# Optimization experiments

Measured on AMD Instinct MI355X. Metric: run time of the kernel, lower is better.

The kernel has to match this reference:

```python
import jax, jax.numpy as jnp
import numpy as np

DIM = 768
HEADS = 12
HEAD_DIM = DIM // HEADS
SEQ = 196
BATCH = 64
SCALE = HEAD_DIM ** -0.5


def setup_inputs() -> dict:
    key = jax.random.key(0)
    ks = jax.random.split(key, 5)
    x = jax.random.normal(ks[0], (BATCH, SEQ, DIM), dtype=jnp.float32)
    W_qkv = jax.random.normal(ks[1], (DIM, 3 * DIM), dtype=jnp.float32) * (DIM ** -0.5)
    static_a = jax.random.truncated_normal(ks[2], -2.0, 2.0, (1, HEADS, SEQ, SEQ), dtype=jnp.float32)
    W_proj = jax.random.normal(ks[3], (DIM, DIM), dtype=jnp.float32) * (DIM ** -0.5)
    b_proj = jnp.zeros((DIM,), dtype=jnp.float32)
    return {"x": x, "W_qkv": W_qkv, "static_a": static_a, "W_proj": W_proj, "b_proj": b_proj}


def reference(x, W_qkv, static_a, W_proj, b_proj):
    B, N, C = x.shape
    qkv = (x @ W_qkv).reshape(B, N, 3, HEADS, HEAD_DIM)
    qkv = jnp.transpose(qkv, (2, 0, 3, 1, 4))  # [3, B, H, N, D]
    q, k, v = qkv[0], qkv[1], qkv[2]
    attn = jnp.einsum('bhnd,bhmd->bhnm', q, k) * SCALE
    attn = jax.nn.softmax(attn, axis=-1) + static_a  # post-softmax additive bias
    out = jnp.einsum('bhnm,bhmd->bhnd', attn, v)  # [B, H, N, D]
    out = jnp.transpose(out, (0, 2, 1, 3)).reshape(B, N, C)
    return out @ W_proj + b_proj
```

## Files before the change

kernel.cpp:

```cpp
#include <hip/hip_runtime.h>
#include <stdint.h>

#define DIM 768
#define HEADS 12
#define SEQ 196
#define BATCH 64
#define NTOK (BATCH*SEQ)
#define SCALE 0.125f

using short8  = __attribute__((ext_vector_type(8))) short;
using short4v = __attribute__((ext_vector_type(4))) short;
using float4v = __attribute__((ext_vector_type(4))) float;
using ushort4v = __attribute__((ext_vector_type(4))) unsigned short;

static __device__ __forceinline__ unsigned short f2bf(float f) {
  union { float f; unsigned u; } v; v.f = f;
  unsigned u = v.u;
  u += 0x7fffu + ((u >> 16) & 1u);
  return (unsigned short)(u >> 16);
}

#if defined(__has_builtin)
#if __has_builtin(__builtin_amdgcn_global_load_lds)
#define HAS_GLL 1
#endif
#endif

static __device__ __forceinline__ void gll16(const unsigned short* g, unsigned short* l) {
#ifdef HAS_GLL
  __builtin_amdgcn_global_load_lds(
      (const __attribute__((address_space(1))) void*)g,
      (__attribute__((address_space(3))) void*)l, 16, 0, 0);
#else
  const int lane = threadIdx.x & 63;
  *(short8*)(l + lane * 8) = *(const short8*)g;
#endif
}

__global__ __launch_bounds__(256) void cast_x_kernel(const float* __restrict__ in,
                                                     unsigned short* __restrict__ out) {
  int i = blockIdx.x * 256 + threadIdx.x;
  float4 v = ((const float4*)in)[i];
  ushort4v o;
  o.x = f2bf(v.x); o.y = f2bf(v.y); o.z = f2bf(v.z); o.w = f2bf(v.w);
  ((ushort4v*)out)[i] = o;
}

__global__ __launch_bounds__(256) void transpose_cast_kernel(const float* __restrict__ in,
                                                             unsigned short* __restrict__ out,
                                                             int R, int C) {
  __shared__ float tile[32][33];
  int c0 = blockIdx.x * 32, r0 = blockIdx.y * 32;
  int tx = threadIdx.x, ty = threadIdx.y;
  for (int i = 0; i < 32; i += 8)
    tile[ty + i][tx] = in[(size_t)(r0 + ty + i) * C + c0 + tx];
  __syncthreads();
  for (int i = 0; i < 32; i += 8)
    out[(size_t)(c0 + ty + i) * R + r0 + tx] = f2bf(tile[tx][ty + i]);
}

template <int MODE>
__global__ __launch_bounds__(256) void gemm_kernel(const unsigned short* __restrict__ A,
                                                   const unsigned short* __restrict__ Bt,
                                                   const float* __restrict__ bias,
                                                   unsigned short* __restrict__ outQKV,
                                                   float* __restrict__ outF) {
  constexpr int K = 768;
  __shared__ __align__(16) unsigned short Als[128 * 32];
  __shared__ __align__(16) unsigned short Bls[128 * 32];
  const int tid = threadIdx.x;
  const int wid = tid >> 6, lane = tid & 63;
  const int s = lane & 15, q = lane >> 4;
  const int wr = wid >> 1, wc = wid & 1;
  const int m0 = blockIdx.y * 128;
  const int n0 = blockIdx.x * 128;

  float4v acc[4][4];
  for (int i = 0; i < 4; i++)
    for (int j = 0; j < 4; j++) acc[i][j] = (float4v){0.f, 0.f, 0.f, 0.f};

  const int srow = lane >> 2;
  const int scol = (lane & 3) * 8;

  for (int kt = 0; kt < K; kt += 32) {
    const unsigned short* ga = A  + (size_t)(m0 + wid * 32 + srow) * K + kt + scol;
    const unsigned short* gb = Bt + (size_t)(n0 + wid * 32 + srow) * K + kt + scol;
    unsigned short* la = &Als[wid * 32 * 32];
    unsigned short* lb = &Bls[wid * 32 * 32];
    gll16(ga,           la);
    gll16(ga + 16 * K,  la + 16 * 32);
    gll16(gb,           lb);
    gll16(gb + 16 * K,  lb + 16 * 32);
    __syncthreads();

    short8 af[4], bf[4];
    for (int i = 0; i < 4; i++)
      af[i] = *(const short8*)&Als[(wr * 64 + i * 16 + s) * 32 + q * 8];
    for (int j = 0; j < 4; j++)
      bf[j] = *(const short8*)&Bls[(wc * 64 + j * 16 + s) * 32 + q * 8];
    for (int i = 0; i < 4; i++)
      for (int j = 0; j < 4; j++)
        acc[i][j] = __builtin_amdgcn_mfma_f32_16x16x32_bf16(af[i], bf[j], acc[i][j], 0, 0, 0);
    __syncthreads();
  }

  for (int i = 0; i < 4; i++) {
    int mbase = m0 + wr * 64 + i * 16 + q * 4;
    for (int j = 0; j < 4; j++) {
      int ng = n0 + wc * 64 + j * 16 + s;
      if (MODE == 0) {
        int t = ng / 768, rem = ng % 768;
        int h = rem >> 6, d = rem & 63;
        for (int r = 0; r < 4; r++) {
          int mg = mbase + r;
          int b = mg / 196, ns = mg - b * 196;
          size_t off = ((size_t)((t * BATCH + b) * HEADS + h) * SEQ + ns) * 64 + d;
          outQKV[off] = f2bf(acc[i][j][r]);
        }
      } else {
        float bv = bias[ng];
        for (int r = 0; r < 4; r++)
          outF[(size_t)(mbase + r) * 768 + ng] = acc[i][j][r] + bv;
      }
    }
  }
}

__global__ __launch_bounds__(256) void attn_kernel(const unsigned short* __restrict__ qkv,
                                                   const float* __restrict__ static_a,
                                                   unsigned short* __restrict__ outA) {
  constexpr int WV = 228;
  __shared__ __align__(16) unsigned short Vt[64 * WV];
  const int tid = threadIdx.x, wid = tid >> 6, lane = tid & 63;
  const int s = lane & 15, q = lane >> 4;
  const int bh = blockIdx.x;
  const int b = bh / 12, h = bh % 12;
  const size_t slab = (size_t)SEQ * 64;
  const unsigned short* Qb = qkv + (size_t)(0 * BATCH * HEADS + bh) * slab;
  const unsigned short* Kb = qkv + (size_t)(1 * BATCH * HEADS + bh) * slab;
  const unsigned short* Vb = qkv + (size_t)(2 * BATCH * HEADS + bh) * slab;

  {
    const int ms = tid & 63;
    const int d0 = (tid >> 6) * 16;
    for (int mb = 0; mb < 4; ++mb) {
      int m = mb * 64 + ms;
      if (m < 224) {
        if (m < 196) {
          short8 v0 = *(const short8*)&Vb[(size_t)m * 64 + d0];
          short8 v1 = *(const short8*)&Vb[(size_t)m * 64 + d0 + 8];
          for (int j = 0; j < 8; j++) Vt[(d0 + j) * WV + m] = (unsigned short)v0[j];
          for (int j = 0; j < 8; j++) Vt[(d0 + 8 + j) * WV + m] = (unsigned short)v1[j];
        } else {
          for (int j = 0; j < 16; j++) Vt[(d0 + j) * WV + m] = 0;
        }
      }
    }
  }
  __syncthreads();

  const int pmbase = (s >> 2) * 8 + (s & 3);

  for (int qt = wid; qt < 13; qt += 4) {
    const int n0 = qt * 16;
    const int nq = n0 + s;
    const int nql = nq > 195 ? 195 : nq;
    short8 qf0 = *(const short8*)&Qb[(size_t)nql * 64 + q * 8];
    short8 qf1 = *(const short8*)&Qb[(size_t)nql * 64 + 32 + q * 8];

    float4v sacc[14];
    for (int tt = 0; tt < 13; tt++) {
      int t = tt >> 1, h4 = tt & 1;
      int m = t * 32 + h4 * 4 + pmbase;
      if (m > 195) m = 195;
      short8 kf0 = *(const short8*)&Kb[(size_t)m * 64 + q * 8];
      short8 kf1 = *(const short8*)&Kb[(size_t)m * 64 + 32 + q * 8];
      float4v z = (float4v){0.f, 0.f, 0.f, 0.f};
      z = __builtin_amdgcn_mfma_f32_16x16x32_bf16(kf0, qf0, z, 0, 0, 0);
      z = __builtin_amdgcn_mfma_f32_16x16x32_bf16(kf1, qf1, z, 0, 0, 0);
      sacc[tt] = z;
    }
    sacc[13] = (float4v){0.f, 0.f, 0.f, 0.f};

    float mx = -3.0e38f;
    for (int tt = 0; tt < 12; tt++)
      for (int i = 0; i < 4; i++) mx = fmaxf(mx, sacc[tt][i]);
    if (q == 0)
      for (int i = 0; i < 4; i++) mx = fmaxf(mx, sacc[12][i]);
    mx = fmaxf(mx, __shfl_xor(mx, 16));
    mx = fmaxf(mx, __shfl_xor(mx, 32));
    const float CE = SCALE * 1.44269504f;
    float sm = 0.f;
    for (int tt = 0; tt < 12; tt++)
      for (int i = 0; i < 4; i++) {
        float e = __builtin_amdgcn_exp2f((sacc[tt][i] - mx) * CE);
        sacc[tt][i] = e; sm += e;
      }
    if (q == 0) {
      for (int i = 0; i < 4; i++) {
        float e = __builtin_amdgcn_exp2f((sacc[12][i] - mx) * CE);
        sacc[12][i] = e; sm += e;
      }
    } else {
      sacc[12] = (float4v){0.f, 0.f, 0.f, 0.f};
    }
    sm += __shfl_xor(sm, 16);
    sm += __shfl_xor(sm, 32);
    const float inv = 1.0f / sm;

    const float* sa = static_a + ((size_t)h * SEQ + nql) * SEQ;
    short8 pfrag[7];
    for (int t = 0; t < 7; t++) {
      short8 pf;
      for (int h4 = 0; h4 < 2; h4++) {
        int tt = 2 * t + h4;
        bool valid = (tt < 12) || (tt == 12 && q == 0);
        float4v a4 = (float4v){0.f, 0.f, 0.f, 0.f};
        if (valid) a4 = *(const float4v*)(sa + t * 32 + q * 8 + h4 * 4);
        int src = valid ? tt : 13;
        for (int i = 0; i < 4; i++) {
          float pv = valid ? (sacc[src][i] * inv + a4[i]) : 0.f;
          pf[h4 * 4 + i] = (short)f2bf(pv);
        }
      }
      pfrag[t] = pf;
    }

    for (int dt = 0; dt < 4; dt++) {
      float4v o = (float4v){0.f, 0.f, 0.f, 0.f};
      for (int t = 0; t < 7; t++) {
        const unsigned short* vp = &Vt[(dt * 16 + s) * WV + t * 32 + q * 8];
        short4v v0 = *(const short4v*)vp;
        short4v v1 = *(const short4v*)(vp + 4);
        short8 vf;
        vf[0] = v0[0]; vf[1] = v0[1]; vf[2] = v0[2]; vf[3] = v0[3];
        vf[4] = v1[0]; vf[5] = v1[1]; vf[6] = v1[2]; vf[7] = v1[3];
        o = __builtin_amdgcn_mfma_f32_16x16x32_bf16(vf, pfrag[t], o, 0, 0, 0);
      }
      if (nq < 196) {
        ushort4v ov;
        ov.x = f2bf(o[0]); ov.y = f2bf(o[1]); ov.z = f2bf(o[2]); ov.w = f2bf(o[3]);
        *(ushort4v*)&outA[((size_t)b * SEQ + nq) * DIM + h * 64 + dt * 16 + q * 4] = ov;
      }
    }
  }
}

extern "C" void kernel_launch(void* const* d_in, const int* in_sizes, int n_in,
                              void* d_out, int out_size, void* d_ws, size_t ws_size,
                              hipStream_t stream) {
  const float* x        = (const float*)d_in[0];
  const float* Wqkv     = (const float*)d_in[1];
  const float* static_a = (const float*)d_in[2];
  const float* Wproj    = (const float*)d_in[3];
  const float* bproj    = (const float*)d_in[4];
  float* out = (float*)d_out;

  unsigned char* ws = (unsigned char*)d_ws;
  size_t off = 0;
  unsigned short* qkv_ws = (unsigned short*)(ws + off); off += (size_t)3 * NTOK * DIM * 2;
  unsigned short* xa_ws  = (unsigned short*)(ws + off); off += (size_t)NTOK * DIM * 2;
  unsigned short* wqkvt  = (unsigned short*)(ws + off); off += (size_t)3 * DIM * DIM * 2;
  unsigned short* wprojt = (unsigned short*)(ws + off); off += (size_t)DIM * DIM * 2;

  cast_x_kernel<<<NTOK * DIM / 4 / 256, 256, 0, stream>>>(x, xa_ws);
  transpose_cast_kernel<<<dim3(3 * DIM / 32, DIM / 32), dim3(32, 8), 0, stream>>>(Wqkv, wqkvt, DIM, 3 * DIM);
  transpose_cast_kernel<<<dim3(DIM / 32, DIM / 32), dim3(32, 8), 0, stream>>>(Wproj, wprojt, DIM, DIM);
  gemm_kernel<0><<<dim3(3 * DIM / 128, NTOK / 128), 256, 0, stream>>>(xa_ws, wqkvt, nullptr, qkv_ws, nullptr);
  attn_kernel<<<BATCH * HEADS, 256, 0, stream>>>(qkv_ws, static_a, xa_ws);
  gemm_kernel<1><<<dim3(DIM / 128, NTOK / 128), 256, 0, stream>>>(xa_ws, wprojt, bproj, nullptr, out);
}
```

Measured before the change: 249.8 us.

## Store QKV row-major with vectorized epilogue and XCD-aware block remap

The QKV GEMM now writes its output in plain token-major [NTOK, 3*DIM] layout. Swapping the MFMA operands lets each lane hold 4 consecutive columns, so the epilogue becomes vectorized 8-byte stores instead of scattered 2-byte writes with div/mod head index math. The attention kernel reads Q/K/V with a row stride of 3*DIM instead of contiguous per-head slabs. Block IDs are also remapped so consecutive tiles land on the same XCD for better L2 reuse, and the global load pointer arithmetic is hoisted out of the K loop. The trade-off is that attention K/Q/V loads become strided across rows, which may reduce their coalescing.

```diff
diff --git a/kernel.cpp b/kernel.cpp
--- a/kernel.cpp
+++ b/kernel.cpp
@@ -6,6 +6,7 @@
 #define SEQ 196
 #define BATCH 64
 #define NTOK (BATCH*SEQ)
+#define QKVLD (3*DIM)
 #define SCALE 0.125f
 
 using short8  = __attribute__((ext_vector_type(8))) short;
@@ -63,7 +64,7 @@
 __global__ __launch_bounds__(256) void gemm_kernel(const unsigned short* __restrict__ A,
                                                    const unsigned short* __restrict__ Bt,
                                                    const float* __restrict__ bias,
-                                                   unsigned short* __restrict__ outQKV,
+                                                   unsigned short* __restrict__ outB,
                                                    float* __restrict__ outF) {
   constexpr int K = 768;
   __shared__ __align__(16) unsigned short Als[128 * 32];
@@ -72,8 +73,18 @@
   const int wid = tid >> 6, lane = tid & 63;
   const int s = lane & 15, q = lane >> 4;
   const int wr = wid >> 1, wc = wid & 1;
-  const int m0 = blockIdx.y * 128;
-  const int n0 = blockIdx.x * 128;
+
+  const int nbx = gridDim.x;
+  const int nb = gridDim.x * gridDim.y;
+  int id = blockIdx.y * nbx + blockIdx.x;
+  {
+    int x = id & 7, lid = id >> 3;
+    int per = nb >> 3, big = nb & 7;
+    id = (x < big) ? x * (per + 1) + lid
+                   : big * (per + 1) + (x - big) * per + lid;
+  }
+  const int m0 = (id / nbx) * 128;
+  const int n0 = (id % nbx) * 128;
 
   float4v acc[4][4];
   for (int i = 0; i < 4; i++)
@@ -82,15 +93,17 @@
   const int srow = lane >> 2;
   const int scol = (lane & 3) * 8;
 
+  const unsigned short* ga = A  + (size_t)(m0 + wid * 32 + srow) * K + scol;
+  const unsigned short* gb = Bt + (size_t)(n0 + wid * 32 + srow) * K + scol;
+  unsigned short* la = &Als[wid * 32 * 32];
+  unsigned short* lb = &Bls[wid * 32 * 32];
+
   for (int kt = 0; kt < K; kt += 32) {
-    const unsigned short* ga = A  + (size_t)(m0 + wid * 32 + srow) * K + kt + scol;
-    const unsigned short* gb = Bt + (size_t)(n0 + wid * 32 + srow) * K + kt + scol;
-    unsigned short* la = &Als[wid * 32 * 32];
-    unsigned short* lb = &Bls[wid * 32 * 32];
     gll16(ga,           la);
     gll16(ga + 16 * K,  la + 16 * 32);
     gll16(gb,           lb);
     gll16(gb + 16 * K,  lb + 16 * 32);
+    ga += 32; gb += 32;
     __syncthreads();
 
     short8 af[4], bf[4];
@@ -99,25 +112,31 @@
     for (int j = 0; j < 4; j++)
       bf[j] = *(const short8*)&Bls[(wc * 64 + j * 16 + s) * 32 + q * 8];
     for (int i = 0; i < 4; i++)
-      for (int j = 0; j < 4; j++)
-        acc[i][j] = __builtin_amdgcn_mfma_f32_16x16x32_bf16(af[i], bf[j], acc[i][j], 0, 0, 0);
+      for (int j = 0; j < 4; j++) {
+        if (MODE == 0)
+          acc[i][j] = __builtin_amdgcn_mfma_f32_16x16x32_bf16(bf[j], af[i], acc[i][j], 0, 0, 0);
+        else
+          acc[i][j] = __builtin_amdgcn_mfma_f32_16x16x32_bf16(af[i], bf[j], acc[i][j], 0, 0, 0);
+      }
     __syncthreads();
   }
 
-  for (int i = 0; i < 4; i++) {
-    int mbase = m0 + wr * 64 + i * 16 + q * 4;
-    for (int j = 0; j < 4; j++) {
-      int ng = n0 + wc * 64 + j * 16 + s;
-      if (MODE == 0) {
-        int t = ng / 768, rem = ng % 768;
-        int h = rem >> 6, d = rem & 63;
-        for (int r = 0; r < 4; r++) {
-          int mg = mbase + r;
-          int b = mg / 196, ns = mg - b * 196;
-          size_t off = ((size_t)((t * BATCH + b) * HEADS + h) * SEQ + ns) * 64 + d;
-          outQKV[off] = f2bf(acc[i][j][r]);
-        }
-      } else {
+  if (MODE == 0) {
+    for (int i = 0; i < 4; i++) {
+      size_t mrow = (size_t)(m0 + wr * 64 + i * 16 + s) * QKVLD;
+      for (int j = 0; j < 4; j++) {
+        int n = n0 + wc * 64 + j * 16 + q * 4;
+        ushort4v ov;
+        ov.x = f2bf(acc[i][j][0]); ov.y = f2bf(acc[i][j][1]);
+        ov.z = f2bf(acc[i][j][2]); ov.w = f2bf(acc[i][j][3]);
+        *(ushort4v*)&outB[mrow + n] = ov;
+      }
+    }
+  } else {
+    for (int i = 0; i < 4; i++) {
+      int mbase = m0 + wr * 64 + i * 16 + q * 4;
+      for (int j = 0; j < 4; j++) {
+        int ng = n0 + wc * 64 + j * 16 + s;
         float bv = bias[ng];
         for (int r = 0; r < 4; r++)
           outF[(size_t)(mbase + r) * 768 + ng] = acc[i][j][r] + bv;
@@ -135,10 +154,9 @@
   const int s = lane & 15, q = lane >> 4;
   const int bh = blockIdx.x;
   const int b = bh / 12, h = bh % 12;
-  const size_t slab = (size_t)SEQ * 64;
-  const unsigned short* Qb = qkv + (size_t)(0 * BATCH * HEADS + bh) * slab;
-  const unsigned short* Kb = qkv + (size_t)(1 * BATCH * HEADS + bh) * slab;
-  const unsigned short* Vb = qkv + (size_t)(2 * BATCH * HEADS + bh) * slab;
+  const unsigned short* Qb = qkv + (size_t)b * SEQ * QKVLD + h * 64;
+  const unsigned short* Kb = Qb + 768;
+  const unsigned short* Vb = Qb + 1536;
 
   {
     const int ms = tid & 63;
@@ -147,8 +165,8 @@
       int m = mb * 64 + ms;
       if (m < 224) {
         if (m < 196) {
-          short8 v0 = *(const short8*)&Vb[(size_t)m * 64 + d0];
-          short8 v1 = *(const short8*)&Vb[(size_t)m * 64 + d0 + 8];
+          short8 v0 = *(const short8*)&Vb[(size_t)m * QKVLD + d0];
+          short8 v1 = *(const short8*)&Vb[(size_t)m * QKVLD + d0 + 8];
           for (int j = 0; j < 8; j++) Vt[(d0 + j) * WV + m] = (unsigned short)v0[j];
           for (int j = 0; j < 8; j++) Vt[(d0 + 8 + j) * WV + m] = (unsigned short)v1[j];
         } else {
@@ -165,16 +183,16 @@
     const int n0 = qt * 16;
     const int nq = n0 + s;
     const int nql = nq > 195 ? 195 : nq;
-    short8 qf0 = *(const short8*)&Qb[(size_t)nql * 64 + q * 8];
-    short8 qf1 = *(const short8*)&Qb[(size_t)nql * 64 + 32 + q * 8];
+    short8 qf0 = *(const short8*)&Qb[(size_t)nql * QKVLD + q * 8];
+    short8 qf1 = *(const short8*)&Qb[(size_t)nql * QKVLD + 32 + q * 8];
 
     float4v sacc[14];
     for (int tt = 0; tt < 13; tt++) {
       int t = tt >> 1, h4 = tt & 1;
       int m = t * 32 + h4 * 4 + pmbase;
       if (m > 195) m = 195;
-      short8 kf0 = *(const short8*)&Kb[(size_t)m * 64 + q * 8];
-      short8 kf1 = *(const short8*)&Kb[(size_t)m * 64 + 32 + q * 8];
+      short8 kf0 = *(const short8*)&Kb[(size_t)m * QKVLD + q * 8];
+      short8 kf1 = *(const short8*)&Kb[(size_t)m * QKVLD + 32 + q * 8];
       float4v z = (float4v){0.f, 0.f, 0.f, 0.f};
       z = __builtin_amdgcn_mfma_f32_16x16x32_bf16(kf0, qf0, z, 0, 0, 0);
       z = __builtin_amdgcn_mfma_f32_16x16x32_bf16(kf1, qf1, z, 0, 0, 0);
@@ -258,7 +276,7 @@
 
   unsigned char* ws = (unsigned char*)d_ws;
   size_t off = 0;
-  unsigned short* qkv_ws = (unsigned short*)(ws + off); off += (size_t)3 * NTOK * DIM * 2;
+  unsigned short* qkv_ws = (unsigned short*)(ws + off); off += (size_t)NTOK * QKVLD * 2;
   unsigned short* xa_ws  = (unsigned short*)(ws + off); off += (size_t)NTOK * DIM * 2;
   unsigned short* wqkvt  = (unsigned short*)(ws + off); off += (size_t)3 * DIM * DIM * 2;
   unsigned short* wprojt = (unsigned short*)(ws + off); off += (size_t)DIM * DIM * 2;
```

New measurement: 249.0 us. About the same (-0.3%).
